# Performance work log

Measured on AMD Instinct MI355X. Metric: run time of the kernel, lower is better.

The kernel has to match this reference:

```python
import jax, jax.numpy as jnp
import numpy as np

B, S, D_IN, D_FF, D_OUT, E = 4, 2048, 1024, 4096, 1024, 8


def setup_inputs() -> dict:
    key = jax.random.key(0)
    ks = jax.random.split(key, 8)
    s = lambda k, shape, fan: jax.random.normal(k, shape, dtype=jnp.float32) * (1.0 / np.sqrt(fan))
    return {
        "x": jax.random.normal(ks[0], (B, S, D_IN), dtype=jnp.float32),
        "switch_w": s(ks[1], (D_IN, E), D_IN),
        "switch_b": jnp.zeros((E,), dtype=jnp.float32),
        "w1": s(ks[2], (E, D_IN, D_FF), D_IN),
        "b1": jnp.zeros((E, D_FF), dtype=jnp.float32),
        "w2": s(ks[3], (E, D_FF, D_OUT), D_FF),
        "b2": jnp.zeros((E, D_OUT), dtype=jnp.float32),
    }


def reference(x, switch_w, switch_b, w1, b1, w2, b2):
    b, s, d = x.shape
    n_experts = w1.shape[0]
    xf = x.reshape(-1, d)                                   # [T, d]
    route_prob = jax.nn.softmax(xf @ switch_w + switch_b, axis=-1)  # [T, E]
    route_prob_max = jnp.max(route_prob, axis=-1)           # [T]
    routes = jnp.argmax(route_prob, axis=-1)                # [T] int, constant wrt grads

    # Per-expert FFN applied to all tokens, combined with top-1 one-hot mask
    # (drop_tokens=False -> every token goes to exactly its argmax expert).
    h = jax.nn.relu(jnp.einsum('td,edf->etf', xf, w1) + b1[:, None, :])   # [E, T, f]
    y_all = jnp.einsum('etf,efo->eto', h, w2) + b2[:, None, :]            # [E, T, d_out]
    onehot = jax.nn.one_hot(routes, n_experts, dtype=xf.dtype)            # [T, E]
    y = jnp.einsum('eto,te->to', y_all, onehot)             # dispatch-combine

    # is_scale_prob=True: scale output by routing probability
    y = y * route_prob_max[:, None]

    counts = onehot.sum(axis=0)                             # tokens per expert
    route_frac = counts / counts.sum()
    aux_loss = n_experts * jnp.sum(route_frac * route_prob.sum(axis=0))

    return y.reshape(b, s, -1), aux_loss
```

## Files before the change

### kernel.cpp

```cpp
#include <hip/hip_runtime.h>
#include <cstdint>
#include <cstddef>

#define NT   8192
#define DIN  1024
#define DFF  4096
#define DOUT 1024
#define NEXP 8

typedef float  f32x4v __attribute__((ext_vector_type(4)));
typedef short  s16x8  __attribute__((ext_vector_type(8)));
typedef short  s16x4  __attribute__((ext_vector_type(4)));

__device__ __forceinline__ ushort f2bf(float f) {
  union { float f; uint32_t u; } c; c.f = f;
  uint32_t u = c.u;
  return (ushort)((u + 0x7fffu + ((u >> 16) & 1u)) >> 16);
}
__device__ __forceinline__ float bf2f(ushort h) {
  union { uint32_t u; float f; } c; c.u = ((uint32_t)h) << 16; return c.f;
}

__global__ __launch_bounds__(256) void router_kernel(
    const float* __restrict__ x, const float* __restrict__ sw,
    const float* __restrict__ sb,
    int* __restrict__ routes, int* __restrict__ posArr,
    float* __restrict__ pmaxArr,
    int* __restrict__ cnt, float* __restrict__ probsum) {
  __shared__ int   sRoute[64];
  __shared__ float sProb[4][NEXP];
  __shared__ int   sBase[NEXP];

  const int lane = threadIdx.x & 63;
  const int w    = threadIdx.x >> 6;
  const int t0   = blockIdx.x * 64;

  float bias[NEXP];
#pragma unroll
  for (int e = 0; e < NEXP; e++) bias[e] = sb[e];

  float wprob[NEXP];
#pragma unroll
  for (int e = 0; e < NEXP; e++) wprob[e] = 0.0f;

  for (int k = 0; k < 16; k++) {
    const int t = t0 + w * 16 + k;
    const float* xr = x + (size_t)t * DIN;
    float acc[NEXP];
#pragma unroll
    for (int e = 0; e < NEXP; e++) acc[e] = 0.0f;
#pragma unroll
    for (int it = 0; it < DIN / 64; it++) {
      const int i = it * 64 + lane;
      const float xv = xr[i];
      const float4 s0 = *(const float4*)(sw + (size_t)i * NEXP);
      const float4 s1 = *(const float4*)(sw + (size_t)i * NEXP + 4);
      acc[0] += xv * s0.x; acc[1] += xv * s0.y; acc[2] += xv * s0.z; acc[3] += xv * s0.w;
      acc[4] += xv * s1.x; acc[5] += xv * s1.y; acc[6] += xv * s1.z; acc[7] += xv * s1.w;
    }
#pragma unroll
    for (int e = 0; e < NEXP; e++) {
#pragma unroll
      for (int off = 32; off > 0; off >>= 1) acc[e] += __shfl_xor(acc[e], off, 64);
    }
    float m = acc[0] + bias[0]; int am = 0;
    float lg[NEXP];
#pragma unroll
    for (int e = 0; e < NEXP; e++) {
      lg[e] = acc[e] + bias[e];
      if (lg[e] > m) { m = lg[e]; am = e; }
    }
    float esum = 0.0f;
    float pe[NEXP];
#pragma unroll
    for (int e = 0; e < NEXP; e++) { pe[e] = __expf(lg[e] - m); esum += pe[e]; }
    const float inv = 1.0f / esum;
#pragma unroll
    for (int e = 0; e < NEXP; e++) wprob[e] += pe[e] * inv;
    if (lane == 0) {
      routes[t] = am;
      pmaxArr[t] = inv;
      sRoute[w * 16 + k] = am;
    }
  }
  if (lane == 0) {
#pragma unroll
    for (int e = 0; e < NEXP; e++) sProb[w][e] = wprob[e];
  }
  __syncthreads();

  const int tid = threadIdx.x;
  if (tid < NEXP) {
    float s = sProb[0][tid] + sProb[1][tid] + sProb[2][tid] + sProb[3][tid];
    atomicAdd(&probsum[tid], s);
    int c = 0;
#pragma unroll
    for (int j = 0; j < 64; j++) c += (sRoute[j] == tid);
    sBase[tid] = atomicAdd(&cnt[tid], c);
  }
  __syncthreads();

  if (tid < 64) {
    const int r = sRoute[tid];
    int rank = 0;
    for (int j = 0; j < 64; j++) rank += (j < tid) & (sRoute[j] == r);
    posArr[t0 + tid] = sBase[r] + rank;
  }
}

__global__ void offsets_aux_kernel(const int* __restrict__ cnt, const float* __restrict__ probsum,
                                   int* __restrict__ offsets, float* __restrict__ auxout) {
  if (threadIdx.x == 0) {
    int o = 0; float aux = 0.0f;
    for (int e = 0; e < NEXP; e++) {
      offsets[e] = o; o += cnt[e];
      aux += (float)cnt[e] * probsum[e];
    }
    offsets[NEXP] = o;
    auxout[0] = aux * ((float)NEXP / (float)NT);
  }
}

__global__ void gather_kernel(const float* __restrict__ x, const int* __restrict__ routes,
                              const int* __restrict__ posArr, const int* __restrict__ offsets,
                              int* __restrict__ perm, ushort* __restrict__ Xg) {
  const int lane = threadIdx.x & 63;
  const int t = (blockIdx.x * blockDim.x + threadIdx.x) >> 6;
  if (t >= NT) return;
  const int slot = offsets[routes[t]] + posArr[t];
  if (lane == 0) perm[slot] = t;
  const float* src = x + (size_t)t * DIN;
  ushort* dst = Xg + (size_t)slot * DIN;
#pragma unroll
  for (int half = 0; half < 2; half++) {
    int i = half * 512 + lane * 8;
    float4 v0 = *(const float4*)(src + i);
    float4 v1 = *(const float4*)(src + i + 4);
    s16x8 p;
    p[0] = (short)f2bf(v0.x); p[1] = (short)f2bf(v0.y);
    p[2] = (short)f2bf(v0.z); p[3] = (short)f2bf(v0.w);
    p[4] = (short)f2bf(v1.x); p[5] = (short)f2bf(v1.y);
    p[6] = (short)f2bf(v1.z); p[7] = (short)f2bf(v1.w);
    *(s16x8*)(dst + i) = p;
  }
}

__global__ void transpose_cvt_kernel(const float* __restrict__ src, ushort* __restrict__ dst,
                                     const int K, const int N) {
  __shared__ float tile[64][65];
  const int ntn = N >> 6;
  const int ntk = K >> 6;
  int b = blockIdx.x;
  const int tn = b % ntn; b /= ntn;
  const int tk = b % ntk; const int e = b / ntk;
  const float* s = src + ((size_t)e * K + (size_t)tk * 64) * N + (size_t)tn * 64;
  const int c4 = (threadIdx.x & 15) * 4;
  const int r0 = threadIdx.x >> 4;
#pragma unroll
  for (int p = 0; p < 4; p++) {
    const int row = r0 + p * 16;
    float4 v = *(const float4*)(s + (size_t)row * N + c4);
    tile[row][c4 + 0] = v.x; tile[row][c4 + 1] = v.y;
    tile[row][c4 + 2] = v.z; tile[row][c4 + 3] = v.w;
  }
  __syncthreads();
  ushort* d = dst + ((size_t)e * N + (size_t)tn * 64) * K + (size_t)tk * 64;
#pragma unroll
  for (int p = 0; p < 4; p++) {
    const int nrow = r0 + p * 16;
    s16x4 o;
    o[0] = (short)f2bf(tile[c4 + 0][nrow]);
    o[1] = (short)f2bf(tile[c4 + 1][nrow]);
    o[2] = (short)f2bf(tile[c4 + 2][nrow]);
    o[3] = (short)f2bf(tile[c4 + 3][nrow]);
    *(s16x4*)(d + (size_t)nrow * K + c4) = o;
  }
}

#define GLD16(g, l)                                                                        \
  __builtin_amdgcn_global_load_lds((const __attribute__((address_space(1))) uint32_t*)(g), \
                                   (__attribute__((address_space(3))) uint32_t*)(l), 16, 0, 0)

#define SBAR()   asm volatile("s_barrier" ::: "memory")
#define WAITV(n) asm volatile("s_waitcnt vmcnt(" #n ")" ::: "memory")

template <int KDIM, int EPI>
__global__ __launch_bounds__(512, 1) void moe_gemm256_kernel(
    const ushort* __restrict__ A,
    const ushort* __restrict__ BT,
    const float* __restrict__ bias,
    const int* __restrict__ offsets,
    ushort* __restrict__ Hout,
    float* __restrict__ Y,
    ushort* __restrict__ P1,
    const int* __restrict__ perm, const float* __restrict__ pmaxArr,
    const int N, const int LDK) {
  __shared__ ushort sA[4][8192];
  __shared__ ushort sB[4][8192];
  int e, bx, by, part;
  if constexpr (EPI == 0) {
    const int logical = ((blockIdx.x & 7) << 7) + (blockIdx.x >> 3);
    e = logical >> 7;
    bx = (logical & 127) >> 3;
    by = logical & 7;
    part = 0;
  } else {
    bx = blockIdx.x; by = blockIdx.y;
    e = blockIdx.z & 7; part = blockIdx.z >> 3;
  }
  const size_t kofs = (size_t)part * KDIM;
  const int mlimit = offsets[e + 1];
  const int m0 = offsets[e] + by * 256;
  if (m0 >= mlimit) return;
  const int n0 = bx * 256;
  const int tid = threadIdx.x;
  const int lane = tid & 63;
  const int wid = tid >> 6;
  const int wr = wid >> 2;
  const int wc = wid & 3;
  const int rsel = lane & 15;
  const int lhi = lane >> 4;

  const int srow = wid * 8 + (lane >> 3);
  const int scol = ((lane & 7) ^ (lane >> 3)) * 8;
  const ushort* gA = A + (size_t)(m0 + srow) * LDK + kofs + scol;
  const ushort* gB = BT + ((size_t)e * N + n0 + srow) * LDK + kofs + scol;
  const int ldst = tid * 8;

#define STAGE_A(s, h, kt)                                                  \
  do {                                                                     \
    const ushort* g_ = gA + (size_t)((h) * 128) * LDK + (size_t)(kt) * 64; \
    GLD16(g_, &sA[s][ldst]);                                               \
    GLD16(g_ + (size_t)64 * LDK, &sA[s][ldst + 4096]);                     \
  } while (0)
#define STAGE_B(s, h, kt)                                                  \
  do {                                                                     \
    const ushort* g_ = gB + (size_t)((h) * 128) * LDK + (size_t)(kt) * 64; \
    GLD16(g_, &sB[s][ldst]);                                               \
    GLD16(g_ + (size_t)64 * LDK, &sB[s][ldst + 4096]);                     \
  } while (0)

  f32x4v acc[2][2][4][2];
#pragma unroll
  for (int i = 0; i < 2; i++)
#pragma unroll
    for (int j = 0; j < 2; j++)
#pragma unroll
      for (int mf = 0; mf < 4; mf++)
#pragma unroll
        for (int nf = 0; nf < 2; nf++) acc[i][j][mf][nf] = (f32x4v)0.0f;

  const int rsw = rsel & 7;
  const int sw0 = ((lhi) ^ rsw) * 8;
  const int sw1 = ((4 + lhi) ^ rsw) * 8;
  int arow[4], brow[2];
#pragma unroll
  for (int mf = 0; mf < 4; mf++) arow[mf] = (wr * 64 + mf * 16 + rsel) * 64;
#pragma unroll
  for (int nf = 0; nf < 2; nf++) brow[nf] = (wc * 32 + nf * 16 + rsel) * 64;

  s16x8 a[4][2], b0[2][2], b1[2][2];

#define LDA(slot)                                                      \
  do {                                                                 \
    _Pragma("unroll") for (int mf = 0; mf < 4; mf++) {                 \
      a[mf][0] = *(const s16x8*)&sA[slot][arow[mf] + sw0];             \
      a[mf][1] = *(const s16x8*)&sA[slot][arow[mf] + sw1];             \
    }                                                                  \
  } while (0)
#define LDB(dst, slot)                                                 \
  do {                                                                 \
    _Pragma("unroll") for (int nf = 0; nf < 2; nf++) {                 \
      dst[nf][0] = *(const s16x8*)&sB[slot][brow[nf] + sw0];           \
      dst[nf][1] = *(const s16x8*)&sB[slot][brow[nf] + sw1];           \
    }                                                                  \
  } while (0)
#define MFMAQ(MG, NG, BB)                                              \
  do {                                                                 \
    __builtin_amdgcn_s_setprio(1);                                     \
    _Pragma("unroll") for (int mf = 0; mf < 4; mf++)                   \
    _Pragma("unroll") for (int nf = 0; nf < 2; nf++)                   \
    _Pragma("unroll") for (int ks = 0; ks < 2; ks++)                   \
      acc[MG][NG][mf][nf] = __builtin_amdgcn_mfma_f32_16x16x32_bf16(   \
          a[mf][ks], BB[nf][ks], acc[MG][NG][mf][nf], 0, 0, 0);        \
    __builtin_amdgcn_s_setprio(0);                                     \
  } while (0)

  constexpr int NS = KDIM / 64;
  STAGE_A(0, 0, 0);
  STAGE_B(0, 0, 0);
  STAGE_B(1, 1, 0);
  STAGE_A(1, 1, 0);
  WAITV(4);
  SBAR();

#pragma unroll 2
  for (int t = 0; t < NS; ++t) {
    const int s0 = (2 * t) & 3, s1 = (2 * t + 1) & 3;
    const int sn0 = (2 * t + 2) & 3, sn1 = (2 * t + 3) & 3;
    const bool more = (t + 1 < NS);
    LDA(s0);
    LDB(b0, s0);
    if (more) { STAGE_A(sn0, 0, t + 1); STAGE_B(sn0, 0, t + 1); }
    SBAR();
    MFMAQ(0, 0, b0);
    if (more) { WAITV(4); } else { WAITV(0); }
    SBAR();
    LDB(b1, s1);
    if (more) STAGE_B(sn1, 1, t + 1);
    SBAR();
    MFMAQ(0, 1, b1);
    SBAR();
    LDA(s1);
    if (more) STAGE_A(sn1, 1, t + 1);
    SBAR();
    MFMAQ(1, 1, b1);
    SBAR();
    MFMAQ(1, 0, b0);
    if (more) { WAITV(4); }
    SBAR();
  }
#undef LDA
#undef LDB
#undef MFMAQ
#undef STAGE_A
#undef STAGE_B

  float bv[2][2];
#pragma unroll
  for (int ng = 0; ng < 2; ng++)
#pragma unroll
    for (int nf = 0; nf < 2; nf++)
      bv[ng][nf] = bias[(size_t)e * N + n0 + ng * 128 + wc * 32 + nf * 16 + rsel];
#pragma unroll
  for (int mg = 0; mg < 2; mg++) {
#pragma unroll
    for (int mf = 0; mf < 4; mf++) {
#pragma unroll
      for (int r = 0; r < 4; r++) {
        const int grow = m0 + mg * 128 + wr * 64 + mf * 16 + lhi * 4 + r;
        if (grow < mlimit) {
          if constexpr (EPI == 0) {
            ushort* hrow = Hout + (size_t)grow * N + n0;
#pragma unroll
            for (int ng = 0; ng < 2; ng++)
#pragma unroll
              for (int nf = 0; nf < 2; nf++) {
                float v = acc[mg][ng][mf][nf][r] + bv[ng][nf];
                hrow[ng * 128 + wc * 32 + nf * 16 + rsel] = f2bf(fmaxf(v, 0.0f));
              }
          } else {
            if (part == 0) {
              const int tok = perm[grow];
              const float sc = pmaxArr[tok];
              float* yrow = Y + (size_t)tok * N + n0;
#pragma unroll
              for (int ng = 0; ng < 2; ng++)
#pragma unroll
                for (int nf = 0; nf < 2; nf++)
                  yrow[ng * 128 + wc * 32 + nf * 16 + rsel] =
                      (acc[mg][ng][mf][nf][r] + bv[ng][nf]) * sc;
            } else {
              ushort* prow = P1 + (size_t)grow * N + n0;
#pragma unroll
              for (int ng = 0; ng < 2; ng++)
#pragma unroll
                for (int nf = 0; nf < 2; nf++)
                  prow[ng * 128 + wc * 32 + nf * 16 + rsel] =
                      f2bf(acc[mg][ng][mf][nf][r]);
            }
          }
        }
      }
    }
  }
}

__global__ __launch_bounds__(256) void combine_kernel(
    const ushort* __restrict__ P1, const int* __restrict__ perm,
    const float* __restrict__ pmaxArr, float* __restrict__ out) {
  const int lane = threadIdx.x & 63;
  const int slot = (blockIdx.x * blockDim.x + threadIdx.x) >> 6;
  if (slot >= NT) return;
  const int tok = perm[slot];
  const float sc = pmaxArr[tok];
  const ushort* src = P1 + (size_t)slot * DOUT;
  float* dst = out + (size_t)tok * DOUT;
#pragma unroll
  for (int half = 0; half < 2; half++) {
    const int i = half * 512 + lane * 8;
    const s16x8 p = *(const s16x8*)(src + i);
    float4 o0 = *(const float4*)(dst + i);
    float4 o1 = *(const float4*)(dst + i + 4);
    o0.x += sc * bf2f((ushort)p[0]); o0.y += sc * bf2f((ushort)p[1]);
    o0.z += sc * bf2f((ushort)p[2]); o0.w += sc * bf2f((ushort)p[3]);
    o1.x += sc * bf2f((ushort)p[4]); o1.y += sc * bf2f((ushort)p[5]);
    o1.z += sc * bf2f((ushort)p[6]); o1.w += sc * bf2f((ushort)p[7]);
    *(float4*)(dst + i) = o0;
    *(float4*)(dst + i + 4) = o1;
  }
}

extern "C" void kernel_launch(void* const* d_in, const int* in_sizes, int n_in,
                              void* d_out, int out_size, void* d_ws, size_t ws_size,
                              hipStream_t stream) {
  const float* x  = (const float*)d_in[0];
  const float* sw = (const float*)d_in[1];
  const float* sb = (const float*)d_in[2];
  const float* w1 = (const float*)d_in[3];
  const float* b1 = (const float*)d_in[4];
  const float* w2 = (const float*)d_in[5];
  const float* b2 = (const float*)d_in[6];
  float* out = (float*)d_out;
  float* auxp = out + (size_t)NT * DOUT;

  char* wsb = (char*)d_ws;
  int*   cnt      = (int*)wsb;
  float* probsum  = (float*)(wsb + 32);
  int*   offsets  = (int*)(wsb + 64);
  int*   routes   = (int*)(wsb + 256);
  int*   posArr   = routes + NT;
  float* pmaxArr  = (float*)(posArr + NT);
  int*   perm     = (int*)(pmaxArr + NT);
  ushort* Xg = (ushort*)(wsb + 256 + (size_t)4 * 4 * NT);
  ushort* Hg = Xg + (size_t)(NT + 256) * DIN;
  ushort* Wt = Hg + (size_t)(NT + 256) * DFF;
  size_t needed = (size_t)((char*)Wt - wsb) + (size_t)NEXP * DFF * DIN * 2;
  if (ws_size < needed) return;
  ushort* P1 = Xg;

  hipMemsetAsync(d_ws, 0, 64, stream);

  router_kernel<<<NT / 64, 256, 0, stream>>>(x, sw, sb, routes, posArr, pmaxArr, cnt, probsum);
  offsets_aux_kernel<<<1, 64, 0, stream>>>(cnt, probsum, offsets, auxp);
  gather_kernel<<<NT / 4, 256, 0, stream>>>(x, routes, posArr, offsets, perm, Xg);

  transpose_cvt_kernel<<<NEXP * (DIN / 64) * (DFF / 64), 256, 0, stream>>>(w1, Wt, DIN, DFF);
  moe_gemm256_kernel<DIN, 0><<<1024, 512, 0, stream>>>(
      Xg, Wt, b1, offsets, Hg, nullptr, nullptr, nullptr, nullptr, DFF, DIN);

  transpose_cvt_kernel<<<NEXP * (DFF / 64) * (DOUT / 64), 256, 0, stream>>>(w2, Wt, DFF, DOUT);
  moe_gemm256_kernel<DFF / 2, 3><<<dim3(DOUT / 256, 10, 16), 512, 0, stream>>>(
      Hg, Wt, b2, offsets, nullptr, out, P1, perm, pmaxArr, DOUT, DFF);
  combine_kernel<<<NT / 4, 256, 0, stream>>>(P1, perm, pmaxArr, out);
}
```

Before: 393.8 us.

## Replace four-slot staged GEMM pipeline with whole-tile double buffering; narrower second-GEMM tiles

```diff
diff --git a/kernel.cpp b/kernel.cpp
--- a/kernel.cpp
+++ b/kernel.cpp
@@ -184,8 +184,8 @@
 #define SBAR()   asm volatile("s_barrier" ::: "memory")
 #define WAITV(n) asm volatile("s_waitcnt vmcnt(" #n ")" ::: "memory")
 
-template <int KDIM, int EPI>
-__global__ __launch_bounds__(512, 1) void moe_gemm256_kernel(
+template <int KDIM, int EPI, int NBH>
+__global__ __launch_bounds__(512, 1) void moe_gemm2p_kernel(
     const ushort* __restrict__ A,
     const ushort* __restrict__ BT,
     const float* __restrict__ bias,
@@ -195,8 +195,8 @@
     ushort* __restrict__ P1,
     const int* __restrict__ perm, const float* __restrict__ pmaxArr,
     const int N, const int LDK) {
-  __shared__ ushort sA[4][8192];
-  __shared__ ushort sB[4][8192];
+  __shared__ ushort sA[2][2][8192];
+  __shared__ ushort sB[2][NBH][8192];
   int e, bx, by, part;
   if constexpr (EPI == 0) {
     const int logical = ((blockIdx.x & 7) << 7) + (blockIdx.x >> 3);
@@ -212,7 +212,7 @@
   const int mlimit = offsets[e + 1];
   const int m0 = offsets[e] + by * 256;
   if (m0 >= mlimit) return;
-  const int n0 = bx * 256;
+  const int n0 = bx * (NBH * 128);
   const int tid = threadIdx.x;
   const int lane = tid & 63;
   const int wid = tid >> 6;
@@ -226,25 +226,29 @@
   const ushort* gA = A + (size_t)(m0 + srow) * LDK + kofs + scol;
   const ushort* gB = BT + ((size_t)e * N + n0 + srow) * LDK + kofs + scol;
   const int ldst = tid * 8;
-
-#define STAGE_A(s, h, kt)                                                  \
-  do {                                                                     \
-    const ushort* g_ = gA + (size_t)((h) * 128) * LDK + (size_t)(kt) * 64; \
-    GLD16(g_, &sA[s][ldst]);                                               \
-    GLD16(g_ + (size_t)64 * LDK, &sA[s][ldst + 4096]);                     \
+  const size_t LK = (size_t)LDK;
+
+#define STAGE_T(buf, kt)                                                \
+  do {                                                                  \
+    const ushort* ga_ = gA + (size_t)(kt) * 64;                         \
+    GLD16(ga_, &sA[buf][0][ldst]);                                      \
+    GLD16(ga_ + 64 * LK, &sA[buf][0][ldst + 4096]);                     \
+    GLD16(ga_ + 128 * LK, &sA[buf][1][ldst]);                           \
+    GLD16(ga_ + 192 * LK, &sA[buf][1][ldst + 4096]);                    \
+    const ushort* gb_ = gB + (size_t)(kt) * 64;                         \
+    GLD16(gb_, &sB[buf][0][ldst]);                                      \
+    GLD16(gb_ + 64 * LK, &sB[buf][0][ldst + 4096]);                     \
+    if (NBH == 2) {                                                     \
+      GLD16(gb_ + 128 * LK, &sB[buf][1][ldst]);                         \
+      GLD16(gb_ + 192 * LK, &sB[buf][1][ldst + 4096]);                  \
+    }                                                                   \
   } while (0)
-#define STAGE_B(s, h, kt)                                                  \
-  do {                                                                     \
-    const ushort* g_ = gB + (size_t)((h) * 128) * LDK + (size_t)(kt) * 64; \
-    GLD16(g_, &sB[s][ldst]);                                               \
-    GLD16(g_ + (size_t)64 * LDK, &sB[s][ldst + 4096]);                     \
-  } while (0)
-
-  f32x4v acc[2][2][4][2];
+
+  f32x4v acc[2][NBH][4][2];
 #pragma unroll
   for (int i = 0; i < 2; i++)
 #pragma unroll
-    for (int j = 0; j < 2; j++)
+    for (int j = 0; j < NBH; j++)
 #pragma unroll
       for (int mf = 0; mf < 4; mf++)
 #pragma unroll
@@ -261,74 +265,63 @@
 
   s16x8 a[4][2], b0[2][2], b1[2][2];
 
-#define LDA(slot)                                                      \
+#define LDA(buf, h)                                                    \
   do {                                                                 \
     _Pragma("unroll") for (int mf = 0; mf < 4; mf++) {                 \
-      a[mf][0] = *(const s16x8*)&sA[slot][arow[mf] + sw0];             \
-      a[mf][1] = *(const s16x8*)&sA[slot][arow[mf] + sw1];             \
+      a[mf][0] = *(const s16x8*)&sA[buf][h][arow[mf] + sw0];           \
+      a[mf][1] = *(const s16x8*)&sA[buf][h][arow[mf] + sw1];           \
     }                                                                  \
   } while (0)
-#define LDB(dst, slot)                                                 \
+#define LDB(dst, buf, h)                                               \
   do {                                                                 \
     _Pragma("unroll") for (int nf = 0; nf < 2; nf++) {                 \
-      dst[nf][0] = *(const s16x8*)&sB[slot][brow[nf] + sw0];           \
-      dst[nf][1] = *(const s16x8*)&sB[slot][brow[nf] + sw1];           \
+      dst[nf][0] = *(const s16x8*)&sB[buf][h][brow[nf] + sw0];         \
+      dst[nf][1] = *(const s16x8*)&sB[buf][h][brow[nf] + sw1];         \
     }                                                                  \
   } while (0)
 #define MFMAQ(MG, NG, BB)                                              \
   do {                                                                 \
-    __builtin_amdgcn_s_setprio(1);                                     \
     _Pragma("unroll") for (int mf = 0; mf < 4; mf++)                   \
     _Pragma("unroll") for (int nf = 0; nf < 2; nf++)                   \
     _Pragma("unroll") for (int ks = 0; ks < 2; ks++)                   \
       acc[MG][NG][mf][nf] = __builtin_amdgcn_mfma_f32_16x16x32_bf16(   \
           a[mf][ks], BB[nf][ks], acc[MG][NG][mf][nf], 0, 0, 0);        \
-    __builtin_amdgcn_s_setprio(0);                                     \
   } while (0)
 
   constexpr int NS = KDIM / 64;
-  STAGE_A(0, 0, 0);
-  STAGE_B(0, 0, 0);
-  STAGE_B(1, 1, 0);
-  STAGE_A(1, 1, 0);
-  WAITV(4);
+  STAGE_T(0, 0);
+  WAITV(0);
   SBAR();
-
-#pragma unroll 2
+  int cur = 0;
   for (int t = 0; t < NS; ++t) {
-    const int s0 = (2 * t) & 3, s1 = (2 * t + 1) & 3;
-    const int sn0 = (2 * t + 2) & 3, sn1 = (2 * t + 3) & 3;
     const bool more = (t + 1 < NS);
-    LDA(s0);
-    LDB(b0, s0);
-    if (more) { STAGE_A(sn0, 0, t + 1); STAGE_B(sn0, 0, t + 1); }
-    SBAR();
+    if (more) STAGE_T(cur ^ 1, t + 1);
+    __builtin_amdgcn_s_setprio(1);
+    LDA(cur, 0);
+    LDB(b0, cur, 0);
     MFMAQ(0, 0, b0);
-    if (more) { WAITV(4); } else { WAITV(0); }
-    SBAR();
-    LDB(b1, s1);
-    if (more) STAGE_B(sn1, 1, t + 1);
-    SBAR();
-    MFMAQ(0, 1, b1);
-    SBAR();
-    LDA(s1);
-    if (more) STAGE_A(sn1, 1, t + 1);
-    SBAR();
-    MFMAQ(1, 1, b1);
-    SBAR();
+    if (NBH == 2) {
+      LDB(b1, cur, 1);
+      MFMAQ(0, 1, b1);
+    }
+    LDA(cur, 1);
+    if (NBH == 2) MFMAQ(1, 1, b1);
     MFMAQ(1, 0, b0);
-    if (more) { WAITV(4); }
-    SBAR();
+    __builtin_amdgcn_s_setprio(0);
+    if (more) {
+      WAITV(0);
+      SBAR();
+      cur ^= 1;
+    }
   }
 #undef LDA
 #undef LDB
 #undef MFMAQ
-#undef STAGE_A
-#undef STAGE_B
-
-  float bv[2][2];
-#pragma unroll
-  for (int ng = 0; ng < 2; ng++)
+#undef STAGE_T
+
+  float bv[NBH][2];
+#pragma unroll
+  for (int ng = 0; ng < NBH; ng++)
 #pragma unroll
     for (int nf = 0; nf < 2; nf++)
       bv[ng][nf] = bias[(size_t)e * N + n0 + ng * 128 + wc * 32 + nf * 16 + rsel];
@@ -343,7 +336,7 @@
           if constexpr (EPI == 0) {
             ushort* hrow = Hout + (size_t)grow * N + n0;
 #pragma unroll
-            for (int ng = 0; ng < 2; ng++)
+            for (int ng = 0; ng < NBH; ng++)
 #pragma unroll
               for (int nf = 0; nf < 2; nf++) {
                 float v = acc[mg][ng][mf][nf][r] + bv[ng][nf];
@@ -355,7 +348,7 @@
               const float sc = pmaxArr[tok];
               float* yrow = Y + (size_t)tok * N + n0;
 #pragma unroll
-              for (int ng = 0; ng < 2; ng++)
+              for (int ng = 0; ng < NBH; ng++)
 #pragma unroll
                 for (int nf = 0; nf < 2; nf++)
                   yrow[ng * 128 + wc * 32 + nf * 16 + rsel] =
@@ -363,7 +356,7 @@
             } else {
               ushort* prow = P1 + (size_t)grow * N + n0;
 #pragma unroll
-              for (int ng = 0; ng < 2; ng++)
+              for (int ng = 0; ng < NBH; ng++)
 #pragma unroll
                 for (int nf = 0; nf < 2; nf++)
                   prow[ng * 128 + wc * 32 + nf * 16 + rsel] =
@@ -436,11 +429,11 @@
   gather_kernel<<<NT / 4, 256, 0, stream>>>(x, routes, posArr, offsets, perm, Xg);
 
   transpose_cvt_kernel<<<NEXP * (DIN / 64) * (DFF / 64), 256, 0, stream>>>(w1, Wt, DIN, DFF);
-  moe_gemm256_kernel<DIN, 0><<<1024, 512, 0, stream>>>(
+  moe_gemm2p_kernel<DIN, 0, 2><<<1024, 512, 0, stream>>>(
       Xg, Wt, b1, offsets, Hg, nullptr, nullptr, nullptr, nullptr, DFF, DIN);
 
   transpose_cvt_kernel<<<NEXP * (DFF / 64) * (DOUT / 64), 256, 0, stream>>>(w2, Wt, DFF, DOUT);
-  moe_gemm256_kernel<DFF / 2, 3><<<dim3(DOUT / 256, 10, 16), 512, 0, stream>>>(
+  moe_gemm2p_kernel<DFF / 2, 3, 1><<<dim3(DOUT / 128, 10, 16), 512, 0, stream>>>(
       Hg, Wt, b2, offsets, nullptr, out, P1, perm, pmaxArr, DOUT, DFF);
   combine_kernel<<<NT / 4, 256, 0, stream>>>(P1, perm, pmaxArr, out);
 }
```

After: 444.1 us. +12.8%, slower.
